# Performance work log

Hardware: AMD Instinct MI355X
Metric: run time of the kernel (lower is better)

Reference implementation:

```python
import jax, jax.numpy as jnp
import numpy as np

CODEBOOK_BITS = 8      # log2(256)
NUM_Q = 2              # NUM_QUANTIZERS
INV_TEMP = 100.0       # LFQ default inv_temperature
DIVERSITY_GAMMA = 1.0
ENTROPY_WEIGHT = 0.1   # LFQ default entropy_loss_weight
COMMIT_WEIGHT = 1.0


def conv2d(x, w, b, pad):
    out = jax.lax.conv_general_dilated(
        x, w, (1, 1), [(pad, pad), (pad, pad)],
        dimension_numbers=('NCHW', 'OIHW', 'NCHW'))
    return out + b[None, :, None, None]


def maxpool2(x):
    return jax.lax.reduce_window(x, -jnp.inf, jax.lax.max,
                                 (1, 1, 2, 2), (1, 1, 2, 2), 'VALID')


def groupnorm(x, groups=4, eps=1e-5):
    B, C, H, W = x.shape
    xg = x.reshape(B, groups, C // groups, H, W)
    mu = xg.mean(axis=(2, 3, 4), keepdims=True)
    var = xg.var(axis=(2, 3, 4), keepdims=True)
    return ((xg - mu) * jax.lax.rsqrt(var + eps)).reshape(B, C, H, W)


def upsample2(x):  # nearest, scale 2
    return jnp.repeat(jnp.repeat(x, 2, axis=2), 2, axis=3)


def lfq_codebook():
    # all 2^8 sign patterns, code j has bit i = ((j>>i)&1)*2-1
    j = jnp.arange(2 ** CODEBOOK_BITS)
    bits = ((j[:, None] >> jnp.arange(CODEBOOK_BITS)[None, :]) & 1).astype(jnp.float32)
    return bits * 2.0 - 1.0  # [256, 8]


def lfq_residual(z):
    # z: (B, D, H, W) with D = CODEBOOK_BITS
    codebook = lfq_codebook()
    t = jnp.transpose(z, (0, 2, 3, 1))  # (B,H,W,D) tokens
    residual = t
    quantized_out = jnp.zeros_like(t)
    pow2 = (2 ** jnp.arange(CODEBOOK_BITS)).astype(jnp.int32)
    indices = []
    aux = jnp.zeros((), t.dtype)
    for _ in range(NUM_Q):
        q_hard = jnp.where(residual > 0, 1.0, -1.0).astype(t.dtype)
        # straight-through binarization
        q = residual + jax.lax.stop_gradient(q_hard - residual)
        idx = jnp.sum((q_hard > 0).astype(jnp.int32) * pow2, axis=-1)  # (B,H,W)
        logits = (2.0 * INV_TEMP) * jnp.einsum('bhwd,cd->bhwc', residual, codebook)
        logp = jax.nn.log_softmax(logits, axis=-1)
        probs = jnp.exp(logp)
        per_sample_entropy = -jnp.mean(jnp.sum(probs * logp, axis=-1))
        avg_prob = jnp.mean(probs.reshape(-1, probs.shape[-1]), axis=0)
        codebook_entropy = -jnp.sum(avg_prob * jnp.log(avg_prob + 1e-10))
        entropy_aux = per_sample_entropy - DIVERSITY_GAMMA * codebook_entropy
        commit = jnp.mean((residual - jax.lax.stop_gradient(q_hard)) ** 2)
        aux = aux + ENTROPY_WEIGHT * entropy_aux + COMMIT_WEIGHT * commit
        quantized_out = quantized_out + q
        residual = residual - jax.lax.stop_gradient(q)
        indices.append(idx)
    q_out = jnp.transpose(quantized_out, (0, 3, 1, 2))  # (B,D,H,W)
    return q_out, jnp.stack(indices, axis=-1), aux


def setup_inputs() -> dict:
    key = jax.random.key(0)
    ks = jax.random.split(key, 13)
    s = 0.05
    return {
        'x': jax.random.normal(ks[0], (32, 1, 256, 256), jnp.float32),
        'w1': jax.random.normal(ks[1], (16, 1, 3, 3), jnp.float32) * s,
        'b1': jax.random.normal(ks[2], (16,), jnp.float32) * s,
        'w2': jax.random.normal(ks[3], (32, 16, 3, 3), jnp.float32) * s,
        'b2': jax.random.normal(ks[4], (32,), jnp.float32) * s,
        'w3': jax.random.normal(ks[5], (8, 32, 1, 1), jnp.float32) * s,
        'b3': jax.random.normal(ks[6], (8,), jnp.float32) * s,
        'd1': jax.random.normal(ks[7], (32, 8, 3, 3), jnp.float32) * s,
        'db1': jax.random.normal(ks[8], (32,), jnp.float32) * s,
        'd2': jax.random.normal(ks[9], (16, 32, 3, 3), jnp.float32) * s,
        'db2': jax.random.normal(ks[10], (16,), jnp.float32) * s,
        'd3': jax.random.normal(ks[11], (1, 16, 3, 3), jnp.float32) * s,
        'db3': jax.random.normal(ks[12], (1,), jnp.float32) * s,
    }


def reference(x, w1, b1, w2, b2, w3, b3, d1, db1, d2, db2, d3, db3):
    # encode
    h = jax.nn.gelu(maxpool2(conv2d(x, w1, b1, pad=1)), approximate=False)
    h = groupnorm(maxpool2(conv2d(h, w2, b2, pad=1)))
    h = conv2d(h, w3, b3, pad=0)  # (B,8,64,64)
    # residual LFQ
    q, indices, aux = lfq_residual(h)
    # decode
    y = upsample2(conv2d(q, d1, db1, pad=1))
    y = upsample2(jax.nn.gelu(conv2d(y, d2, db2, pad=1), approximate=False))
    y = conv2d(y, d3, db3, pad=1)
    return jnp.clip(y, -1.0, 1.0), indices, aux
```

## Files before the change

### kernel.cpp

```cpp
#include <hip/hip_runtime.h>
#include <hip/hip_bf16.h>
#include <math.h>

#define DEV __device__ __forceinline__

DEV float gelu_exact(float x){ return 0.5f*x*(1.0f + erff(x*0.70710678118654752f)); }

__global__ __launch_bounds__(256) void k_prep(const float* __restrict__ w2,
    const float* __restrict__ d2, float* __restrict__ w2t, float* __restrict__ wp4d2)
{
  const int gid = blockIdx.x*256 + threadIdx.x;
  for(int i=gid;i<4608;i+=2048){
    int oc=i/144, rem=i-oc*144, ic=rem/9, k=rem-ic*9;
    w2t[(ic*32+oc)*9+k]=w2[i];
  }
  for(int i=gid;i<2048;i+=2048){
    int par=i>>9, ic=(i>>4)&31, oc=i&15;
    int py=par>>1, px=par&1;
    const float* wg = d2 + ((size_t)oc*32+ic)*9;
    float a00=0.f,a01=0.f,a10=0.f,a11=0.f;
    #pragma unroll
    for(int ky=0;ky<3;ky++){
      int sy = py ? (ky>>1) : ((ky>0)?1:0);
      #pragma unroll
      for(int kx=0;kx<3;kx++){
        int sx = px ? (kx>>1) : ((kx>0)?1:0);
        float wv=wg[ky*3+kx];
        if(sy==0){ if(sx==0)a00+=wv; else a01+=wv; }
        else     { if(sx==0)a10+=wv; else a11+=wv; }
      }
    }
    float* dst=wp4d2+(size_t)i*4;
    dst[0]=a00; dst[1]=a01; dst[2]=a10; dst[3]=a11;
  }
}

__global__ __launch_bounds__(256) void k_conv1(const float* __restrict__ x,
    const float* __restrict__ w1, const float* __restrict__ b1,
    float* __restrict__ h1)
{
  __shared__ float sE[34*19], sO[34*19];
  const int b = blockIdx.z;
  const int r0 = blockIdx.x*32, c0 = blockIdx.y*32;
  const float* xp = x + (size_t)b*65536;
  for(int i=threadIdx.x;i<34*34;i+=256){
    int r=i/34, c=i-r*34;
    int gr=r0+r-1, gc=c0+c-1;
    float v=0.f;
    if(gr>=0 && gr<256 && gc>=0 && gc<256) v = xp[gr*256+gc];
    if(c&1) sO[r*19+(c>>1)]=v; else sE[r*19+(c>>1)]=v;
  }
  __syncthreads();
  const int tx=threadIdx.x&15, ty=threadIdx.x>>4;
  const int base = 2*ty*19 + tx;
  float in[4][4];
  #pragma unroll
  for(int r=0;r<4;r++){
    in[r][0]=sE[base+r*19]; in[r][1]=sO[base+r*19];
    in[r][2]=sE[base+r*19+1]; in[r][3]=sO[base+r*19+1];
  }
  const int py = blockIdx.x*16+ty, px = blockIdx.y*16+tx;
  float* op = h1 + ((size_t)b*16)*16384 + py*128 + px;
  #pragma unroll
  for(int ch=0;ch<16;ch++){
    float m=-1e30f;
    #pragma unroll
    for(int pr=0;pr<2;pr++)
      #pragma unroll
      for(int pc=0;pc<2;pc++){
        float a=0.f;
        #pragma unroll
        for(int ky=0;ky<3;ky++)
          #pragma unroll
          for(int kx=0;kx<3;kx++)
            a = fmaf(in[pr+ky][pc+kx], w1[ch*9+ky*3+kx], a);
        m = fmaxf(m,a);
      }
    op[(size_t)ch*16384] = gelu_exact(m + b1[ch]);
  }
}

__global__ __launch_bounds__(256) void k_conv2(const float* __restrict__ h1,
    const float* __restrict__ w2t, const float* __restrict__ b2,
    float* __restrict__ h2, double* __restrict__ pb)
{
  __shared__ __align__(16) float t2[8*360];
  const int b=blockIdx.z;
  const int r0=blockIdx.x*16, c0=blockIdx.y*16;
  const float* hp = h1 + (size_t)b*16*16384;
  const int pos=threadIdx.x&63;
  const int ocg=__builtin_amdgcn_readfirstlane((int)(threadIdx.x>>6));
  const int oc0=ocg*8;
  const int pyl=pos>>3, pxl=pos&7;
  const int base0 = 2*pyl*20 + 2*pxl;
  float acc[8][4];
  #pragma unroll
  for(int o=0;o<8;o++)
    #pragma unroll
    for(int j=0;j<4;j++) acc[o][j]=0.f;

  for(int half=0;half<2;half++){
    for(int i=threadIdx.x;i<1296;i+=256){
      int ic=i/162, rem=i-ic*162, lr=rem/9, jp=rem-lr*9;
      int gr=r0+lr-1, gc=c0+2*jp-1;
      float v0=0.f, v1=0.f;
      if(gr>=0&&gr<128){
        const float* row=hp+(size_t)(half*8+ic)*16384+(size_t)gr*128;
        if(gc>=0&&gc<128) v0=row[gc];
        if(gc+1<128)      v1=row[gc+1];
      }
      *(float2*)&t2[ic*360+lr*20+2*jp]=make_float2(v0,v1);
    }
    __syncthreads();
    #pragma unroll 4
    for(int ic=0;ic<8;ic++){
      float in[4][4];
      #pragma unroll
      for(int r=0;r<4;r++){
        float2 a=*(const float2*)&t2[ic*360 + base0 + r*20];
        float2 c=*(const float2*)&t2[ic*360 + base0 + r*20 + 2];
        in[r][0]=a.x; in[r][1]=a.y; in[r][2]=c.x; in[r][3]=c.y;
      }
      const float* wp = w2t + ((half*8+ic)*32+oc0)*9;
      #pragma unroll
      for(int o=0;o<8;o++){
        #pragma unroll
        for(int pr=0;pr<2;pr++)
          #pragma unroll
          for(int pc=0;pc<2;pc++){
            float s=acc[o][pr*2+pc];
            #pragma unroll
            for(int ky=0;ky<3;ky++)
              #pragma unroll
              for(int kx=0;kx<3;kx++)
                s=fmaf(in[pr+ky][pc+kx], wp[o*9+ky*3+kx], s);
            acc[o][pr*2+pc]=s;
          }
      }
    }
    __syncthreads();
  }
  const int py=blockIdx.x*8+pyl, px=blockIdx.y*8+pxl;
  double s=0.0, s2=0.0;
  #pragma unroll
  for(int o=0;o<8;o++){
    const int oc=oc0+o;
    float m=fmaxf(fmaxf(acc[o][0],acc[o][1]),fmaxf(acc[o][2],acc[o][3]));
    float hv=m+b2[oc];
    h2[(((size_t)b*32+oc)*64+py)*64+px]=hv;
    s += (double)hv; s2 += (double)hv*(double)hv;
  }
  #pragma unroll
  for(int off=32;off;off>>=1){
    s  += __shfl_xor(s,  off, 64);
    s2 += __shfl_xor(s2, off, 64);
  }
  if(pos==0){
    const int bidx = blockIdx.x*8 + blockIdx.y;
    double* p = pb + (((size_t)b*4+ocg)*64 + bidx)*2;
    p[0]=s; p[1]=s2;
  }
}

__global__ __launch_bounds__(64) void k_stats2(const double* __restrict__ pb,
                                               float* __restrict__ stats)
{
  const int bg=blockIdx.x, t=threadIdx.x;
  double s = pb[((size_t)bg*64+t)*2], s2 = pb[((size_t)bg*64+t)*2+1];
  #pragma unroll
  for(int off=32;off;off>>=1){
    s  += __shfl_xor(s,  off, 64);
    s2 += __shfl_xor(s2, off, 64);
  }
  if(t==0){
    double mu=s/32768.0;
    double var=s2/32768.0 - mu*mu;
    stats[bg]=(float)mu;
    stats[128+bg]=(float)(1.0/sqrt(var+1e-5));
  }
}

__global__ __launch_bounds__(256) void k_lfq(const float* __restrict__ h2,
    const float* __restrict__ stats, const float* __restrict__ w3, const float* __restrict__ b3,
    float* __restrict__ qout, float* __restrict__ idxout,
    float* __restrict__ avgp, float* __restrict__ ec)
{
  __shared__ __align__(16) float tabL[16*258];
  __shared__ __align__(16) float tabH[16*258];
  const int blk=blockIdx.x;
  const int b=blk>>4;
  const int t=threadIdx.x;
  const int h=(blk&15)*4 + (t>>6);
  const int w=t&63;
  float mu[4], rs[4];
  #pragma unroll
  for(int g=0;g<4;g++){ mu[g]=stats[b*4+g]; rs[g]=stats[128+b*4+g]; }
  const float* hp = h2 + (size_t)b*131072 + h*64 + w;
  float z[8];
  #pragma unroll
  for(int d=0;d<8;d++) z[d]=b3[d];
  #pragma unroll
  for(int c=0;c<32;c++){
    float xn=(hp[(size_t)c*4096]-mu[c>>3])*rs[c>>3];
    #pragma unroll
    for(int d=0;d<8;d++) z[d]=fmaf(xn, w3[d*32+c], z[d]);
  }
  float r[8], qsum[8];
  #pragma unroll
  for(int d=0;d<8;d++){ r[d]=z[d]; qsum[d]=0.f; }
  float entk[2], comk[2];
  #pragma unroll
  for(int k=0;k<2;k++){
    int idx=0; float ent=0.f, com=0.f;
    float pb0[8], pb1[8];
    #pragma unroll
    for(int d=0;d<8;d++){
      float rv=r[d];
      bool pos = rv>0.f;
      float sgn = pos?1.f:-1.f;
      idx |= (pos?1:0)<<d;
      float dd=rv-sgn; com=fmaf(dd,dd,com);
      float a=400.f*fabsf(rv);
      float e=__expf(-a);
      float p=1.f/(1.f+e);
      ent += a - p*a - __logf(p);
      float pm=p, pq=1.f-p;
      pb1[d]=pos?pm:pq;
      pb0[d]=pos?pq:pm;
      qsum[d]+=sgn;
      r[d]=rv-sgn;
    }
    float lo[16], hi[16];
    lo[0]=pb0[0]; lo[1]=pb1[0];
    lo[2]=lo[0]*pb1[1]; lo[3]=lo[1]*pb1[1]; lo[0]*=pb0[1]; lo[1]*=pb0[1];
    lo[4]=lo[0]*pb1[2]; lo[5]=lo[1]*pb1[2]; lo[6]=lo[2]*pb1[2]; lo[7]=lo[3]*pb1[2];
    lo[0]*=pb0[2]; lo[1]*=pb0[2]; lo[2]*=pb0[2]; lo[3]*=pb0[2];
    lo[8]=lo[0]*pb1[3]; lo[9]=lo[1]*pb1[3]; lo[10]=lo[2]*pb1[3]; lo[11]=lo[3]*pb1[3];
    lo[12]=lo[4]*pb1[3]; lo[13]=lo[5]*pb1[3]; lo[14]=lo[6]*pb1[3]; lo[15]=lo[7]*pb1[3];
    lo[0]*=pb0[3]; lo[1]*=pb0[3]; lo[2]*=pb0[3]; lo[3]*=pb0[3];
    lo[4]*=pb0[3]; lo[5]*=pb0[3]; lo[6]*=pb0[3]; lo[7]*=pb0[3];
    hi[0]=pb0[4]; hi[1]=pb1[4];
    hi[2]=hi[0]*pb1[5]; hi[3]=hi[1]*pb1[5]; hi[0]*=pb0[5]; hi[1]*=pb0[5];
    hi[4]=hi[0]*pb1[6]; hi[5]=hi[1]*pb1[6]; hi[6]=hi[2]*pb1[6]; hi[7]=hi[3]*pb1[6];
    hi[0]*=pb0[6]; hi[1]*=pb0[6]; hi[2]*=pb0[6]; hi[3]*=pb0[6];
    hi[8]=hi[0]*pb1[7]; hi[9]=hi[1]*pb1[7]; hi[10]=hi[2]*pb1[7]; hi[11]=hi[3]*pb1[7];
    hi[12]=hi[4]*pb1[7]; hi[13]=hi[5]*pb1[7]; hi[14]=hi[6]*pb1[7]; hi[15]=hi[7]*pb1[7];
    hi[0]*=pb0[7]; hi[1]*=pb0[7]; hi[2]*=pb0[7]; hi[3]*=pb0[7];
    hi[4]*=pb0[7]; hi[5]*=pb0[7]; hi[6]*=pb0[7]; hi[7]*=pb0[7];
    #pragma unroll
    for(int m=0;m<16;m++){ tabL[m*258+t]=lo[m]; tabH[m*258+t]=hi[m]; }
    __syncthreads();
    float accp=0.f, accq=0.f;
    const int jl=t&15, jh=t>>4;
    const float* Lp=&tabL[jl*258];
    const float* Hp=&tabH[jh*258];
    #pragma unroll 8
    for(int q=0;q<128;q++){
      float2 L=*(const float2*)&Lp[2*q];
      float2 H=*(const float2*)&Hp[2*q];
      accp=fmaf(L.x,H.x,accp); accq=fmaf(L.y,H.y,accq);
    }
    avgp[((size_t)k*512+blk)*256+t]=accp+accq;
    __syncthreads();
    entk[k]=ent; comk[k]=com;
    idxout[((size_t)(b*64+h)*64+w)*2+k]=(float)idx;
  }
  #pragma unroll
  for(int d=0;d<8;d++)
    qout[(((size_t)b*8+d)*64+h)*64+w]=qsum[d];
  tabL[t]=entk[0]; tabL[256+t]=entk[1]; tabL[512+t]=comk[0]; tabL[768+t]=comk[1];
  __syncthreads();
  for(int st=128;st>0;st>>=1){
    if(t<st){ tabL[t]+=tabL[t+st]; tabL[256+t]+=tabL[256+t+st];
              tabL[512+t]+=tabL[512+t+st]; tabL[768+t]+=tabL[768+t+st]; }
    __syncthreads();
  }
  if(t==0){ ec[blk*4+0]=tabL[0]; ec[blk*4+1]=tabL[256]; ec[blk*4+2]=tabL[512]; ec[blk*4+3]=tabL[768]; }
}

__global__ __launch_bounds__(256) void k_red(const float* __restrict__ avgp,
    float* __restrict__ avgs)
{
  const int k=blockIdx.x>>4, c0=(blockIdx.x&15)*16;
  const int col=threadIdx.x&15, rg=threadIdx.x>>4;
  float s=0.f;
  for(int j=0;j<32;j++){
    int blk=rg+16*j;
    s+=avgp[((size_t)k*512+blk)*256+c0+col];
  }
  __shared__ float red[256];
  red[threadIdx.x]=s; __syncthreads();
  for(int st=128;st>=16;st>>=1){
    if(threadIdx.x<st) red[threadIdx.x]+=red[threadIdx.x+st];
    __syncthreads();
  }
  if(threadIdx.x<16) avgs[k*256+c0+threadIdx.x]=red[threadIdx.x];
}

__global__ __launch_bounds__(256) void k_final(const float* __restrict__ avgs,
    const float* __restrict__ ec, float* __restrict__ auxout)
{
  __shared__ double red[256];
  const int t=threadIdx.x;
  double cb=0.0;
  #pragma unroll
  for(int k=0;k<2;k++){
    double ap=(double)avgs[k*256+t]*(1.0/131072.0);
    cb += -(ap*log(ap+1e-10));
  }
  red[t]=cb; __syncthreads();
  for(int st=128;st>0;st>>=1){ if(t<st) red[t]+=red[t+st]; __syncthreads(); }
  double CB=red[0]; __syncthreads();
  double e=0.0,c=0.0;
  for(int blk=t;blk<512;blk+=256){
    e += (double)ec[blk*4+0]+(double)ec[blk*4+1];
    c += (double)ec[blk*4+2]+(double)ec[blk*4+3];
  }
  red[t]=e; __syncthreads();
  for(int st=128;st>0;st>>=1){ if(t<st) red[t]+=red[t+st]; __syncthreads(); }
  double E=red[0]; __syncthreads();
  red[t]=c; __syncthreads();
  for(int st=128;st>0;st>>=1){ if(t<st) red[t]+=red[t+st]; __syncthreads(); }
  if(t==0){
    double C=red[0];
    double aux = 0.1*(E*(1.0/131072.0) - CB) + C*(1.0/1048576.0);
    auxout[0]=(float)aux;
  }
}

__global__ __launch_bounds__(256) void k_dec1(const float* __restrict__ q,
    const float* __restrict__ d1, const float* __restrict__ db1, float* __restrict__ out1)
{
  __shared__ float tile[8*110];
  const int b=blockIdx.z, r0=blockIdx.x*8, c0=blockIdx.y*8;
  const float* qp = q + (size_t)b*8*4096;
  for(int i=threadIdx.x;i<800;i+=256){
    int ic=i/100, rem=i-ic*100, r=rem/10, c=rem-r*10;
    int gr=r0+r-1, gc=c0+c-1;
    float v=0.f;
    if(gr>=0&&gr<64&&gc>=0&&gc<64) v=qp[ic*4096+gr*64+gc];
    tile[ic*110+r*11+c]=v;
  }
  __syncthreads();
  const int ocg=__builtin_amdgcn_readfirstlane((int)(threadIdx.x>>6));
  const int oc0=ocg*8;
  const int l=threadIdx.x&63, ry=l>>3, cx=l&7;
  float acc[8];
  #pragma unroll
  for(int o=0;o<8;o++) acc[o]=db1[oc0+o];
  #pragma unroll 2
  for(int ic=0;ic<8;ic++){
    float v[9];
    #pragma unroll
    for(int ky=0;ky<3;ky++)
      #pragma unroll
      for(int kx=0;kx<3;kx++)
        v[ky*3+kx]=tile[ic*110+(ry+ky)*11+cx+kx];
    #pragma unroll
    for(int o=0;o<8;o++){
      const float* wp=&d1[((oc0+o)*8+ic)*9];
      float s=acc[o];
      #pragma unroll
      for(int kk=0;kk<9;kk++) s=fmaf(v[kk],wp[kk],s);
      acc[o]=s;
    }
  }
  #pragma unroll
  for(int o=0;o<8;o++)
    out1[(((size_t)b*32+oc0+o)*64 + r0+ry)*64 + c0+cx]=acc[o];
}

__global__ __launch_bounds__(256) void k_dec2(const float* __restrict__ out1,
    const float* __restrict__ wp4d2, const float* __restrict__ db2, float* __restrict__ out2)
{
  __shared__ float tile[32*110];
  const int b=blockIdx.z, y0=blockIdx.x*16, x0=blockIdx.y*16;
  const int sy0=(y0>>1)-1, sx0=(x0>>1)-1;
  const float* sp = out1 + (size_t)b*32*4096;
  for(int i=threadIdx.x;i<3200;i+=256){
    int ic=i/100, rem=i-ic*100, r=rem/10, c=rem-r*10;
    int gr=sy0+r, gc=sx0+c;
    float v=0.f;
    if(gr>=0&&gr<64&&gc>=0&&gc<64) v=sp[ic*4096+gr*64+gc];
    tile[ic*110+r*11+c]=v;
  }
  __syncthreads();
  const int par=__builtin_amdgcn_readfirstlane((int)(threadIdx.x>>6));
  const int py=par>>1, px=par&1;
  const int l=threadIdx.x&63, ry=l>>3, cx=l&7;
  const int byl=ry+py, bxl=cx+px;
  float acc[16];
  #pragma unroll
  for(int o=0;o<16;o++) acc[o]=db2[o];
  #pragma unroll 2
  for(int ic=0;ic<32;ic++){
    const float* tp=&tile[ic*110 + byl*11 + bxl];
    const float s00=tp[0], s01=tp[1], s10=tp[11], s11=tp[12];
    const float* wq = wp4d2 + (size_t)((par*32+ic)*16)*4;
    #pragma unroll
    for(int o=0;o<16;o++)
      acc[o]=fmaf(s00,wq[o*4],fmaf(s01,wq[o*4+1],fmaf(s10,wq[o*4+2],fmaf(s11,wq[o*4+3],acc[o]))));
  }
  const int Y=y0+2*ry+py, X=x0+2*cx+px;
  #pragma unroll
  for(int o=0;o<16;o++)
    out2[((size_t)b*16+o)*16384 + (size_t)Y*128 + X] = gelu_exact(acc[o]);
}

__global__ __launch_bounds__(256) void k_dec3(const float* __restrict__ out2,
    const float* __restrict__ d3, const float* __restrict__ db3, float* __restrict__ y)
{
  __shared__ float tile[16*342];
  __shared__ float4 wp4[64];
  const int b=blockIdx.z, y0=blockIdx.x*32, x0=blockIdx.y*32;
  const int sy0=(y0>>1)-1, sx0=(x0>>1)-1;
  const float* sp = out2 + (size_t)b*16*16384;
  for(int i=threadIdx.x;i<16*324;i+=256){
    int ic=i/324, rem=i-ic*324, r=rem/18, c=rem-r*18;
    int gr=sy0+r, gc=sx0+c;
    float v=0.f;
    if(gr>=0&&gr<128&&gc>=0&&gc<128) v=sp[ic*16384+gr*128+gc];
    tile[ic*342+r*19+c]=v;
  }
  if(threadIdx.x<64){
    int par=threadIdx.x>>4, ic=threadIdx.x&15;
    int py=par>>1, px=par&1;
    const float* wg = d3 + ic*9;
    float a00=0.f,a01=0.f,a10=0.f,a11=0.f;
    #pragma unroll
    for(int ky=0;ky<3;ky++){
      int sy = py ? (ky>>1) : ((ky>0)?1:0);
      #pragma unroll
      for(int kx=0;kx<3;kx++){
        int sx = px ? (kx>>1) : ((kx>0)?1:0);
        float wv=wg[ky*3+kx];
        if(sy==0){ if(sx==0)a00+=wv; else a01+=wv; }
        else     { if(sx==0)a10+=wv; else a11+=wv; }
      }
    }
    wp4[threadIdx.x]=make_float4(a00,a01,a10,a11);
  }
  __syncthreads();
  const float bias=db3[0];
  const int par=__builtin_amdgcn_readfirstlane((int)(threadIdx.x>>6));
  const int py=par>>1, px=par&1;
  const int l=threadIdx.x&63, r0l=l>>4, cl=l&15;
  const int bxl=cl+px;
  float acc[4];
  #pragma unroll
  for(int a=0;a<4;a++) acc[a]=bias;
  #pragma unroll 2
  for(int ic=0;ic<16;ic++){
    const float4 wv=wp4[par*16+ic];
    #pragma unroll
    for(int a=0;a<4;a++){
      const int byl=r0l+4*a+py;
      const float* tp=&tile[ic*342 + byl*19 + bxl];
      acc[a]=fmaf(tp[0],wv.x,fmaf(tp[1],wv.y,fmaf(tp[19],wv.z,fmaf(tp[20],wv.w,acc[a]))));
    }
  }
  #pragma unroll
  for(int a=0;a<4;a++){
    const int yy=2*(r0l+4*a)+py, xx=2*cl+px;
    float v=fminf(fmaxf(acc[a],-1.0f),1.0f);
    y[(size_t)b*65536 + (size_t)(y0+yy)*256 + (x0+xx)] = v;
  }
}

extern "C" void kernel_launch(void* const* d_in, const int* in_sizes, int n_in,
                              void* d_out, int out_size, void* d_ws, size_t ws_size,
                              hipStream_t stream)
{
  const float* x  =(const float*)d_in[0];
  const float* w1 =(const float*)d_in[1];
  const float* b1 =(const float*)d_in[2];
  const float* w2 =(const float*)d_in[3];
  const float* b2 =(const float*)d_in[4];
  const float* w3 =(const float*)d_in[5];
  const float* b3 =(const float*)d_in[6];
  const float* d1 =(const float*)d_in[7];
  const float* db1=(const float*)d_in[8];
  const float* d2 =(const float*)d_in[9];
  const float* db2=(const float*)d_in[10];
  const float* d3 =(const float*)d_in[11];
  const float* db3=(const float*)d_in[12];
  float* out=(float*)d_out;
  float* ws =(float*)d_ws;
  float* h1   = ws;
  float* h2   = ws + 8388608;
  float* qb   = ws + 12582912;
  float* st   = ws + 13631488;
  float* avgp = ws + 13631744;
  float* ec   = ws + 13893888;
  float* w2t  = avgp;
  float* wp4d2= ws + 13895936;
  float* avgs = ws + 13904128;
  double* pb  = (double*)qb;
  float* out1 = h2;
  float* out2 = h1;

  k_prep  <<<dim3(8),256,0,stream>>>(w2,d2,w2t,wp4d2);
  k_conv1 <<<dim3(8,8,32),256,0,stream>>>(x,w1,b1,h1);
  k_conv2 <<<dim3(8,8,32),256,0,stream>>>(h1,w2t,b2,h2,pb);
  k_stats2<<<dim3(128),64,0,stream>>>(pb,st);
  k_lfq   <<<dim3(512),256,0,stream>>>(h2,st,w3,b3,qb,out+2097152,avgp,ec);
  k_red   <<<dim3(32),256,0,stream>>>(avgp,avgs);
  k_final <<<dim3(1),256,0,stream>>>(avgs,ec,out+2359296);
  k_dec1  <<<dim3(8,8,32),256,0,stream>>>(qb,d1,db1,out1);
  k_dec2  <<<dim3(8,8,32),256,0,stream>>>(out1,wp4d2,db2,out2);
  k_dec3  <<<dim3(8,8,32),256,0,stream>>>(out2,d3,db3,out);
}
```

Baseline: 202.3 us.

## Fuse conv1 into conv2 with halo recompute, fold prep and stats into consumers

Merges the first conv+pool+gelu stage into the second conv kernel. Each block recomputes its 18x18 halo of h1 for all 16 channels in shared memory, so the h1 intermediate no longer goes through global memory. The d2 weight prep moves into a few conv blocks, and the GroupNorm stats reduction moves into the LFQ kernel, which removes three launches. The LFQ table reduction now uses float4 loads with padding changed to 260. The cost is redundant conv1 work on halo pixels, more shared memory per block, and pb now living in the output buffer until the decoder overwrites it.

```diff
diff --git a/kernel.cpp b/kernel.cpp
--- a/kernel.cpp
+++ b/kernel.cpp
@@ -6,90 +6,70 @@
 
 DEV float gelu_exact(float x){ return 0.5f*x*(1.0f + erff(x*0.70710678118654752f)); }
 
-__global__ __launch_bounds__(256) void k_prep(const float* __restrict__ w2,
-    const float* __restrict__ d2, float* __restrict__ w2t, float* __restrict__ wp4d2)
-{
-  const int gid = blockIdx.x*256 + threadIdx.x;
-  for(int i=gid;i<4608;i+=2048){
-    int oc=i/144, rem=i-oc*144, ic=rem/9, k=rem-ic*9;
-    w2t[(ic*32+oc)*9+k]=w2[i];
-  }
-  for(int i=gid;i<2048;i+=2048){
-    int par=i>>9, ic=(i>>4)&31, oc=i&15;
-    int py=par>>1, px=par&1;
-    const float* wg = d2 + ((size_t)oc*32+ic)*9;
-    float a00=0.f,a01=0.f,a10=0.f,a11=0.f;
-    #pragma unroll
-    for(int ky=0;ky<3;ky++){
-      int sy = py ? (ky>>1) : ((ky>0)?1:0);
-      #pragma unroll
-      for(int kx=0;kx<3;kx++){
-        int sx = px ? (kx>>1) : ((kx>0)?1:0);
-        float wv=wg[ky*3+kx];
-        if(sy==0){ if(sx==0)a00+=wv; else a01+=wv; }
-        else     { if(sx==0)a10+=wv; else a11+=wv; }
-      }
-    }
-    float* dst=wp4d2+(size_t)i*4;
-    dst[0]=a00; dst[1]=a01; dst[2]=a10; dst[3]=a11;
-  }
-}
-
-__global__ __launch_bounds__(256) void k_conv1(const float* __restrict__ x,
+__global__ __launch_bounds__(256) void k_conv12(const float* __restrict__ x,
     const float* __restrict__ w1, const float* __restrict__ b1,
-    float* __restrict__ h1)
-{
-  __shared__ float sE[34*19], sO[34*19];
-  const int b = blockIdx.z;
-  const int r0 = blockIdx.x*32, c0 = blockIdx.y*32;
-  const float* xp = x + (size_t)b*65536;
-  for(int i=threadIdx.x;i<34*34;i+=256){
-    int r=i/34, c=i-r*34;
-    int gr=r0+r-1, gc=c0+c-1;
-    float v=0.f;
-    if(gr>=0 && gr<256 && gc>=0 && gc<256) v = xp[gr*256+gc];
-    if(c&1) sO[r*19+(c>>1)]=v; else sE[r*19+(c>>1)]=v;
-  }
-  __syncthreads();
-  const int tx=threadIdx.x&15, ty=threadIdx.x>>4;
-  const int base = 2*ty*19 + tx;
-  float in[4][4];
-  #pragma unroll
-  for(int r=0;r<4;r++){
-    in[r][0]=sE[base+r*19]; in[r][1]=sO[base+r*19];
-    in[r][2]=sE[base+r*19+1]; in[r][3]=sO[base+r*19+1];
-  }
-  const int py = blockIdx.x*16+ty, px = blockIdx.y*16+tx;
-  float* op = h1 + ((size_t)b*16)*16384 + py*128 + px;
-  #pragma unroll
-  for(int ch=0;ch<16;ch++){
-    float m=-1e30f;
-    #pragma unroll
-    for(int pr=0;pr<2;pr++)
-      #pragma unroll
-      for(int pc=0;pc<2;pc++){
-        float a=0.f;
-        #pragma unroll
-        for(int ky=0;ky<3;ky++)
-          #pragma unroll
-          for(int kx=0;kx<3;kx++)
-            a = fmaf(in[pr+ky][pc+kx], w1[ch*9+ky*3+kx], a);
-        m = fmaxf(m,a);
-      }
-    op[(size_t)ch*16384] = gelu_exact(m + b1[ch]);
-  }
-}
-
-__global__ __launch_bounds__(256) void k_conv2(const float* __restrict__ h1,
-    const float* __restrict__ w2t, const float* __restrict__ b2,
+    const float* __restrict__ w2, const float* __restrict__ b2,
+    const float* __restrict__ d2, float* __restrict__ wp4d2,
     float* __restrict__ h2, double* __restrict__ pb)
 {
-  __shared__ __align__(16) float t2[8*360];
+  __shared__ float xs[38*40];
+  __shared__ __align__(16) float t2[16*360];
   const int b=blockIdx.z;
   const int r0=blockIdx.x*16, c0=blockIdx.y*16;
-  const float* hp = h1 + (size_t)b*16*16384;
-  const int pos=threadIdx.x&63;
-  const int ocg=__builtin_amdgcn_readfirstlane((int)(threadIdx.x>>6));
+  const int t=threadIdx.x;
+  const float* xp = x + (size_t)b*65536;
+  const int xr0=2*r0-3, xc0=2*c0-3;
+  for(int i=t;i<1444;i+=256){
+    int r=i/38, c=i-38*r;
+    int gr=xr0+r, gc=xc0+c;
+    float v=0.f;
+    if(gr>=0&&gr<256&&gc>=0&&gc<256) v=xp[gr*256+gc];
+    xs[r*40+c]=v;
+  }
+  __syncthreads();
+  {
+    const int wv=__builtin_amdgcn_readfirstlane((int)(t>>6));
+    const int ln=t&63;
+    #pragma unroll
+    for(int ii=0;ii<4;ii++){
+      const int ic=wv+4*ii;
+      #pragma unroll 2
+      for(int s=0;s<6;s++){
+        int j=ln+64*s;
+        if(j<324){
+          int lr=j/18, lc=j-18*lr;
+          int py=r0-1+lr, px=c0-1+lc;
+          float hv=0.f;
+          if(((unsigned)py<128u)&&((unsigned)px<128u)){
+            float in[4][4];
+            #pragma unroll
+            for(int r=0;r<4;r++)
+              #pragma unroll
+              for(int c=0;c<4;c++)
+                in[r][c]=xs[(2*lr+r)*40 + 2*lc + c];
+            float m=-1e30f;
+            #pragma unroll
+            for(int pr=0;pr<2;pr++)
+              #pragma unroll
+              for(int pc=0;pc<2;pc++){
+                float a=0.f;
+                #pragma unroll
+                for(int ky=0;ky<3;ky++)
+                  #pragma unroll
+                  for(int kx=0;kx<3;kx++)
+                    a=fmaf(in[pr+ky][pc+kx], w1[ic*9+ky*3+kx], a);
+                m=fmaxf(m,a);
+              }
+            hv=gelu_exact(m+b1[ic]);
+          }
+          t2[ic*360+lr*20+lc]=hv;
+        }
+      }
+    }
+  }
+  __syncthreads();
+  const int pos=t&63;
+  const int ocg=__builtin_amdgcn_readfirstlane((int)(t>>6));
   const int oc0=ocg*8;
   const int pyl=pos>>3, pxl=pos&7;
   const int base0 = 2*pyl*20 + 2*pxl;
@@ -98,47 +78,31 @@
   for(int o=0;o<8;o++)
     #pragma unroll
     for(int j=0;j<4;j++) acc[o][j]=0.f;
-
-  for(int half=0;half<2;half++){
-    for(int i=threadIdx.x;i<1296;i+=256){
-      int ic=i/162, rem=i-ic*162, lr=rem/9, jp=rem-lr*9;
-      int gr=r0+lr-1, gc=c0+2*jp-1;
-      float v0=0.f, v1=0.f;
-      if(gr>=0&&gr<128){
-        const float* row=hp+(size_t)(half*8+ic)*16384+(size_t)gr*128;
-        if(gc>=0&&gc<128) v0=row[gc];
-        if(gc+1<128)      v1=row[gc+1];
-      }
-      *(float2*)&t2[ic*360+lr*20+2*jp]=make_float2(v0,v1);
-    }
-    __syncthreads();
-    #pragma unroll 4
-    for(int ic=0;ic<8;ic++){
-      float in[4][4];
+  #pragma unroll 4
+  for(int ic=0;ic<16;ic++){
+    float in[4][4];
+    #pragma unroll
+    for(int r=0;r<4;r++){
+      float2 a=*(const float2*)&t2[ic*360 + base0 + r*20];
+      float2 c=*(const float2*)&t2[ic*360 + base0 + r*20 + 2];
+      in[r][0]=a.x; in[r][1]=a.y; in[r][2]=c.x; in[r][3]=c.y;
+    }
+    #pragma unroll
+    for(int o=0;o<8;o++){
+      const float* wp = w2 + ((size_t)(oc0+o)*16+ic)*9;
       #pragma unroll
-      for(int r=0;r<4;r++){
-        float2 a=*(const float2*)&t2[ic*360 + base0 + r*20];
-        float2 c=*(const float2*)&t2[ic*360 + base0 + r*20 + 2];
-        in[r][0]=a.x; in[r][1]=a.y; in[r][2]=c.x; in[r][3]=c.y;
-      }
-      const float* wp = w2t + ((half*8+ic)*32+oc0)*9;
-      #pragma unroll
-      for(int o=0;o<8;o++){
+      for(int pr=0;pr<2;pr++)
         #pragma unroll
-        for(int pr=0;pr<2;pr++)
+        for(int pc=0;pc<2;pc++){
+          float s=acc[o][pr*2+pc];
           #pragma unroll
-          for(int pc=0;pc<2;pc++){
-            float s=acc[o][pr*2+pc];
+          for(int ky=0;ky<3;ky++)
             #pragma unroll
-            for(int ky=0;ky<3;ky++)
-              #pragma unroll
-              for(int kx=0;kx<3;kx++)
-                s=fmaf(in[pr+ky][pc+kx], wp[o*9+ky*3+kx], s);
-            acc[o][pr*2+pc]=s;
-          }
-      }
-    }
-    __syncthreads();
+            for(int kx=0;kx<3;kx++)
+              s=fmaf(in[pr+ky][pc+kx], wp[ky*3+kx], s);
+          acc[o][pr*2+pc]=s;
+        }
+    }
   }
   const int py=blockIdx.x*8+pyl, px=blockIdx.y*8+pxl;
   double s=0.0, s2=0.0;
@@ -160,41 +124,63 @@
     double* p = pb + (((size_t)b*4+ocg)*64 + bidx)*2;
     p[0]=s; p[1]=s2;
   }
-}
-
-__global__ __launch_bounds__(64) void k_stats2(const double* __restrict__ pb,
-                                               float* __restrict__ stats)
-{
-  const int bg=blockIdx.x, t=threadIdx.x;
-  double s = pb[((size_t)bg*64+t)*2], s2 = pb[((size_t)bg*64+t)*2+1];
-  #pragma unroll
-  for(int off=32;off;off>>=1){
-    s  += __shfl_xor(s,  off, 64);
-    s2 += __shfl_xor(s2, off, 64);
-  }
-  if(t==0){
-    double mu=s/32768.0;
-    double var=s2/32768.0 - mu*mu;
-    stats[bg]=(float)mu;
-    stats[128+bg]=(float)(1.0/sqrt(var+1e-5));
+  if(blockIdx.x==0 && blockIdx.y==0 && b<8){
+    const int gid = b*256 + t;
+    for(int i=gid;i<2048;i+=2048){
+      int par=i>>9, ic=(i>>4)&31, oc=i&15;
+      int pyp=par>>1, pxp=par&1;
+      const float* wg = d2 + ((size_t)oc*32+ic)*9;
+      float a00=0.f,a01=0.f,a10=0.f,a11=0.f;
+      #pragma unroll
+      for(int ky=0;ky<3;ky++){
+        int sy = pyp ? (ky>>1) : ((ky>0)?1:0);
+        #pragma unroll
+        for(int kx=0;kx<3;kx++){
+          int sx = pxp ? (kx>>1) : ((kx>0)?1:0);
+          float wv=wg[ky*3+kx];
+          if(sy==0){ if(sx==0)a00+=wv; else a01+=wv; }
+          else     { if(sx==0)a10+=wv; else a11+=wv; }
+        }
+      }
+      float* dst=wp4d2+(size_t)i*4;
+      dst[0]=a00; dst[1]=a01; dst[2]=a10; dst[3]=a11;
+    }
   }
 }
 
 __global__ __launch_bounds__(256) void k_lfq(const float* __restrict__ h2,
-    const float* __restrict__ stats, const float* __restrict__ w3, const float* __restrict__ b3,
+    const double* __restrict__ pb, const float* __restrict__ w3, const float* __restrict__ b3,
     float* __restrict__ qout, float* __restrict__ idxout,
     float* __restrict__ avgp, float* __restrict__ ec)
 {
-  __shared__ __align__(16) float tabL[16*258];
-  __shared__ __align__(16) float tabH[16*258];
+  __shared__ __align__(16) float tabL[16*260];
+  __shared__ __align__(16) float tabH[16*260];
+  __shared__ float smu[4], srs[4];
   const int blk=blockIdx.x;
   const int b=blk>>4;
   const int t=threadIdx.x;
   const int h=(blk&15)*4 + (t>>6);
   const int w=t&63;
+  {
+    const int wv=t>>6, ln=t&63;
+    double s = pb[(((size_t)b*4+wv)*64+ln)*2];
+    double s2= pb[(((size_t)b*4+wv)*64+ln)*2+1];
+    #pragma unroll
+    for(int off=32;off;off>>=1){
+      s  += __shfl_xor(s,  off, 64);
+      s2 += __shfl_xor(s2, off, 64);
+    }
+    if(ln==0){
+      double mu=s/32768.0;
+      double var=s2/32768.0 - mu*mu;
+      smu[wv]=(float)mu;
+      srs[wv]=(float)(1.0/sqrt(var+1e-5));
+    }
+  }
+  __syncthreads();
   float mu[4], rs[4];
   #pragma unroll
-  for(int g=0;g<4;g++){ mu[g]=stats[b*4+g]; rs[g]=stats[128+b*4+g]; }
+  for(int g=0;g<4;g++){ mu[g]=smu[g]; rs[g]=srs[g]; }
   const float* hp = h2 + (size_t)b*131072 + h*64 + w;
   float z[8];
   #pragma unroll
@@ -248,17 +234,18 @@
     hi[0]*=pb0[7]; hi[1]*=pb0[7]; hi[2]*=pb0[7]; hi[3]*=pb0[7];
     hi[4]*=pb0[7]; hi[5]*=pb0[7]; hi[6]*=pb0[7]; hi[7]*=pb0[7];
     #pragma unroll
-    for(int m=0;m<16;m++){ tabL[m*258+t]=lo[m]; tabH[m*258+t]=hi[m]; }
+    for(int m=0;m<16;m++){ tabL[m*260+t]=lo[m]; tabH[m*260+t]=hi[m]; }
     __syncthreads();
     float accp=0.f, accq=0.f;
     const int jl=t&15, jh=t>>4;
-    const float* Lp=&tabL[jl*258];
-    const float* Hp=&tabH[jh*258];
-    #pragma unroll 8
-    for(int q=0;q<128;q++){
-      float2 L=*(const float2*)&Lp[2*q];
-      float2 H=*(const float2*)&Hp[2*q];
+    const float* Lp=&tabL[jl*260];
+    const float* Hp=&tabH[jh*260];
+    #pragma unroll 4
+    for(int q4=0;q4<64;q4++){
+      float4 L=*(const float4*)&Lp[4*q4];
+      float4 H=*(const float4*)&Hp[4*q4];
       accp=fmaf(L.x,H.x,accp); accq=fmaf(L.y,H.y,accq);
+      accp=fmaf(L.z,H.z,accp); accq=fmaf(L.w,H.w,accq);
     }
     avgp[((size_t)k*512+blk)*256+t]=accp+accq;
     __syncthreads();
@@ -486,24 +473,18 @@
   const float* db3=(const float*)d_in[12];
   float* out=(float*)d_out;
   float* ws =(float*)d_ws;
-  float* h1   = ws;
   float* h2   = ws + 8388608;
   float* qb   = ws + 12582912;
-  float* st   = ws + 13631488;
   float* avgp = ws + 13631744;
   float* ec   = ws + 13893888;
-  float* w2t  = avgp;
   float* wp4d2= ws + 13895936;
   float* avgs = ws + 13904128;
-  double* pb  = (double*)qb;
+  double* pb  = (double*)out;
   float* out1 = h2;
-  float* out2 = h1;
-
-  k_prep  <<<dim3(8),256,0,stream>>>(w2,d2,w2t,wp4d2);
-  k_conv1 <<<dim3(8,8,32),256,0,stream>>>(x,w1,b1,h1);
-  k_conv2 <<<dim3(8,8,32),256,0,stream>>>(h1,w2t,b2,h2,pb);
-  k_stats2<<<dim3(128),64,0,stream>>>(pb,st);
-  k_lfq   <<<dim3(512),256,0,stream>>>(h2,st,w3,b3,qb,out+2097152,avgp,ec);
+  float* out2 = ws;
+
+  k_conv12<<<dim3(8,8,32),256,0,stream>>>(x,w1,b1,w2,b2,d2,wp4d2,h2,pb);
+  k_lfq   <<<dim3(512),256,0,stream>>>(h2,pb,w3,b3,qb,out+2097152,avgp,ec);
   k_red   <<<dim3(32),256,0,stream>>>(avgp,avgs);
   k_final <<<dim3(1),256,0,stream>>>(avgs,ec,out+2359296);
   k_dec1  <<<dim3(8,8,32),256,0,stream>>>(qb,d1,db1,out1);
```

Result: slower. 285.3 us (+41.0%).
